# Optimization experiments

Measured on AMD Instinct MI355X. Metric: run time of the kernel, lower is better.

## Reference

```python
import jax, jax.numpy as jnp
import numpy as np

B = 32; H = 56; W = 56; DIM = 384; HEADS = 12; WIN = 7; SHIFT = 3
HEAD_DIM = DIM // HEADS; SCALE = HEAD_DIM ** -0.5
N = WIN * WIN; NW = (H // WIN) * (W // WIN); L = H * W + 1; HID = 4 * DIM


def _rel_index():
    coords = np.stack(np.meshgrid(np.arange(WIN), np.arange(WIN), indexing='ij')).reshape(2, -1)
    rel = (coords[:, :, None] - coords[:, None, :]).transpose(1, 2, 0)
    rel[:, :, 0] += WIN - 1
    rel[:, :, 1] += WIN - 1
    rel[:, :, 0] *= 2 * WIN - 1
    return jnp.asarray(rel.sum(-1))  # (N, N) int


def _attn_mask():
    # standard Swin shift mask, padded with a zero column so the cls key is always visible
    img = np.zeros((H, W))
    sl = (slice(0, -WIN), slice(-WIN, -SHIFT), slice(-SHIFT, None))
    cnt = 0
    for hs in sl:
        for ws in sl:
            img[hs, ws] = cnt
            cnt += 1
    mw = img.reshape(H // WIN, WIN, W // WIN, WIN).transpose(0, 2, 1, 3).reshape(-1, N)
    m = mw[:, None, :] - mw[:, :, None]
    m = np.where(m != 0, -100.0, 0.0).astype(np.float32)
    m = np.pad(m, ((0, 0), (0, 0), (1, 0)))  # (nW, N, N+1)
    return jnp.asarray(m)


REL_INDEX = _rel_index()
ATTN_MASK = _attn_mask()


def _ln(x, g, b, eps=1e-5):
    m = x.mean(-1, keepdims=True)
    v = ((x - m) ** 2).mean(-1, keepdims=True)
    return (x - m) * jax.lax.rsqrt(v + eps) * g + b


def setup_inputs() -> dict:
    key = jax.random.key(0)
    ks = jax.random.split(key, 6)
    s = 0.02
    return dict(
        x=jax.random.normal(ks[0], (B, L, DIM), jnp.float32),
        norm1_g=jnp.ones((DIM,), jnp.float32), norm1_b=jnp.zeros((DIM,), jnp.float32),
        qkv_w=jax.random.normal(ks[1], (3 * DIM, DIM), jnp.float32) * s,
        qkv_b=jnp.zeros((3 * DIM,), jnp.float32),
        rel_bias_table=jax.random.normal(ks[2], ((2 * WIN - 1) ** 2, HEADS), jnp.float32) * s,
        proj_w=jax.random.normal(ks[3], (DIM, DIM), jnp.float32) * s,
        proj_b=jnp.zeros((DIM,), jnp.float32),
        norm2_g=jnp.ones((DIM,), jnp.float32), norm2_b=jnp.zeros((DIM,), jnp.float32),
        fc1_w=jax.random.normal(ks[4], (HID, DIM), jnp.float32) * s,
        fc1_b=jnp.zeros((HID,), jnp.float32),
        fc2_w=jax.random.normal(ks[5], (DIM, HID), jnp.float32) * s,
        fc2_b=jnp.zeros((DIM,), jnp.float32),
    )


def reference(x, norm1_g, norm1_b, qkv_w, qkv_b, rel_bias_table, proj_w, proj_b,
              norm2_g, norm2_b, fc1_w, fc1_b, fc2_w, fc2_b):
    Bx = x.shape[0]
    shortcut = x
    h = _ln(x, norm1_g, norm1_b)
    qkv = h @ qkv_w.T + qkv_b  # (B, L, 3C)

    # ---- global cls attention: token 0 attends to every token (ClsAttention) ----
    t = qkv.reshape(Bx, L, 3, HEADS, HEAD_DIM).transpose(2, 0, 3, 1, 4)  # (3, B, h, L, d)
    q0 = t[0, :, :, 0:1, :] * SCALE
    cls_attn = jax.nn.softmax(jnp.einsum('bhqd,bhkd->bhqk', q0, t[1]), axis=-1)
    cls_out = jnp.einsum('bhqk,bhkd->bhqd', cls_attn, t[2]).transpose(0, 2, 1, 3).reshape(Bx, 1, DIM)

    # ---- shifted-window attention for patch tokens, cls qkv prepended per window ----
    cls_qkv = qkv[:, :1]  # (B, 1, 3C)
    p = qkv[:, 1:].reshape(Bx, H, W, 3 * DIM)
    p = jnp.roll(p, (-SHIFT, -SHIFT), axis=(1, 2))
    pw = p.reshape(Bx, H // WIN, WIN, W // WIN, WIN, 3 * DIM).transpose(0, 1, 3, 2, 4, 5)
    pw = pw.reshape(Bx * NW, N, 3 * DIM)
    cls_rep = jnp.broadcast_to(cls_qkv[:, None], (Bx, NW, 1, 3 * DIM)).reshape(Bx * NW, 1, 3 * DIM)
    qkvw = jnp.concatenate([cls_rep, pw], axis=1)  # (B*nW, N+1, 3C)

    tw = qkvw.reshape(Bx * NW, N + 1, 3, HEADS, HEAD_DIM).transpose(2, 0, 3, 1, 4)
    q = tw[0, :, :, 1:, :] * SCALE  # patch queries (B*nW, h, N, d)
    attn = jnp.einsum('bhqd,bhkd->bhqk', q, tw[1])  # (B*nW, h, N, N+1)
    rel = rel_bias_table[REL_INDEX.reshape(-1)].reshape(N, N, HEADS).transpose(2, 0, 1)
    attn = jnp.concatenate([attn[..., :1], attn[..., 1:] + rel[None]], axis=-1)
    attn = attn.reshape(Bx, NW, HEADS, N, N + 1) + ATTN_MASK[None, :, None]
    attn = jax.nn.softmax(attn.reshape(Bx * NW, HEADS, N, N + 1), axis=-1)
    xw = jnp.einsum('bhqk,bhkd->bhqd', attn, tw[2]).transpose(0, 2, 1, 3).reshape(Bx * NW, N, DIM)

    # window reverse + reverse cyclic shift
    xp = xw.reshape(Bx, H // WIN, W // WIN, WIN, WIN, DIM).transpose(0, 1, 3, 2, 4, 5).reshape(Bx, H, W, DIM)
    xp = jnp.roll(xp, (SHIFT, SHIFT), axis=(1, 2)).reshape(Bx, H * W, DIM)

    a = jnp.concatenate([cls_out, xp], axis=1) @ proj_w.T + proj_b
    x1 = shortcut + a
    h2 = _ln(x1, norm2_g, norm2_b)
    h2 = jax.nn.gelu(h2 @ fc1_w.T + fc1_b, approximate=False)
    return x1 + (h2 @ fc2_w.T + fc2_b)
```

## Files before the change

kernel.cpp:

```cpp
#include <hip/hip_runtime.h>

#define DEVI __device__ __forceinline__

typedef __attribute__((ext_vector_type(8))) __bf16 bf16x8;
typedef __attribute__((ext_vector_type(4))) float f32x4;
typedef unsigned short u16;
typedef unsigned int u32;

static constexpr int kB = 32;
static constexpr int kL = 3137;
static constexpr int kM = kB * kL;
static constexpr int kHeads = 12;
static constexpr float kScale = 0.17677669529663687f;
static constexpr int kNC = 13;

DEVI u16 f2b(float f) {
  u32 u = __float_as_uint(f);
  u32 r = (u + 0x7fffu + ((u >> 16) & 1u)) >> 16;
  return (u16)r;
}
DEVI float blo(u32 u) { return __uint_as_float(u << 16); }
DEVI float bhi(u32 u) { return __uint_as_float(u & 0xffff0000u); }
DEVI float b2f(u16 h) { return __uint_as_float(((u32)h) << 16); }

DEVI void async16(const void* g, void* l) {
  __builtin_amdgcn_global_load_lds((const __attribute__((address_space(1))) u32*)g,
                                   (__attribute__((address_space(3))) u32*)l, 16, 0, 0);
}

DEVI float wred_max(float v) {
#pragma unroll
  for (int o = 32; o; o >>= 1) v = fmaxf(v, __shfl_xor(v, o));
  return v;
}
DEVI float wred_sum(float v) {
#pragma unroll
  for (int o = 32; o; o >>= 1) v += __shfl_xor(v, o);
  return v;
}

__global__ void cvt_all(const float* __restrict__ a, const float* __restrict__ b,
                        const float* __restrict__ c2, const float* __restrict__ d,
                        u16* __restrict__ oa, u16* __restrict__ ob,
                        u16* __restrict__ oc, u16* __restrict__ od) {
  int i = blockIdx.x * 256 + threadIdx.x;
  if (i < 442368) oa[i] = f2b(a[i]);
  else if (i < 589824) ob[i - 442368] = f2b(b[i - 442368]);
  else if (i < 1179648) oc[i - 589824] = f2b(c2[i - 589824]);
  else od[i - 1179648] = f2b(d[i - 1179648]);
}

__global__ __launch_bounds__(256)
void ln384(const float* __restrict__ x, const float* __restrict__ gam,
           const float* __restrict__ bet, u16* __restrict__ out, int rows) {
  int row = blockIdx.x * 4 + (threadIdx.x >> 6);
  if (row >= rows) return;
  int lane = threadIdx.x & 63;
  const float2* xr = (const float2*)(x + (size_t)row * 384);
  float2 v[3];
  float s = 0.f, s2 = 0.f;
#pragma unroll
  for (int i = 0; i < 3; i++) {
    v[i] = xr[lane + 64 * i];
    s += v[i].x + v[i].y;
    s2 += v[i].x * v[i].x + v[i].y * v[i].y;
  }
  s = wred_sum(s);
  s2 = wred_sum(s2);
  float mean = s * (1.f / 384.f);
  float var = s2 * (1.f / 384.f) - mean * mean;
  float rinv = rsqrtf(var + 1e-5f);
  const float2* gp = (const float2*)gam;
  const float2* bp = (const float2*)bet;
  u32* orow = (u32*)(out + (size_t)row * 384);
#pragma unroll
  for (int i = 0; i < 3; i++) {
    int idx = lane + 64 * i;
    float2 gg = gp[idx], bb = bp[idx];
    float lo = (v[i].x - mean) * rinv * gg.x + bb.x;
    float hi = (v[i].y - mean) * rinv * gg.y + bb.y;
    orow[idx] = (u32)f2b(lo) | ((u32)f2b(hi) << 16);
  }
}

DEVI float gelu_exact(float v) { return 0.5f * v * (1.f + erff(v * 0.70710678118654752f)); }

template <int EPI>
__global__ __launch_bounds__(256)
void gemm_bt(const u16* __restrict__ A, const u16* __restrict__ W,
             const float* __restrict__ bias, const float* __restrict__ res,
             void* __restrict__ outp, int M, int N, int K, int NX, int TMv) {
  const int nwg = gridDim.x;
  const int orig = blockIdx.x;
  const int xcd = orig & 7, rest = orig >> 3;
  const int q8 = nwg >> 3, r8 = nwg & 7;
  const int id = ((xcd < r8) ? xcd * (q8 + 1) : r8 * (q8 + 1) + (xcd - r8) * q8) + rest;
  const int col0 = (id % NX) * 128;
  const int rowG = (id / NX) * TMv * 128;

  const int tid = threadIdx.x, lane = tid & 63, wv = tid >> 6;
  __shared__ __align__(16) u16 As[3][128 * 32];
  __shared__ __align__(16) u16 Bs[3][128 * 32];
  const int wm = wv >> 1, wn = wv & 1;
  const int c = lane & 15, g = lane >> 4;
  const int NT = K >> 5;

  const int rr = lane >> 2;
  const int gnat = (lane & 3) ^ ((lane >> 3) & 3);

  auto stage = [&](int t2, int k2, int bfi) {
    int kk = k2 * 32 + gnat * 8;
    int rbase = rowG + t2 * 128;
#pragma unroll
    for (int s = 0; s < 2; s++) {
      int ch = wv * 2 + s;
      int r = ch * 16 + rr;
      async16(A + (size_t)min(rbase + r, M - 1) * K + kk, &As[bfi][ch * 512]);
      async16(W + (size_t)min(col0 + r, N - 1) * K + kk, &Bs[bfi][ch * 512]);
    }
  };

  int cc[4];
  float bv[4];
#pragma unroll
  for (int n = 0; n < 4; n++) {
    cc[n] = col0 + wn * 64 + n * 16 + c;
    bv[n] = bias[cc[n]];
  }

  stage(0, 0, 0);
  stage(0, 1, 1);
  int cur = 0;
  for (int t = 0; t < TMv; ++t) {
    f32x4 acc[4][4];
    f32x4 zero = {0.f, 0.f, 0.f, 0.f};
#pragma unroll
    for (int m = 0; m < 4; m++)
#pragma unroll
      for (int n = 0; n < 4; n++) acc[m][n] = zero;

    for (int kt = 0; kt < NT; ++kt) {
      if (t == TMv - 1 && kt == NT - 1) asm volatile("s_waitcnt vmcnt(0)" ::: "memory");
      else                              asm volatile("s_waitcnt vmcnt(4)" ::: "memory");
      __builtin_amdgcn_s_barrier();
      {
        int kt2 = kt + 2, t2 = t;
        if (kt2 >= NT) { kt2 -= NT; t2++; }
        if (t2 < TMv) {
          int nb = cur + 2; if (nb >= 3) nb -= 3;
          stage(t2, kt2, nb);
        }
      }
      bf16x8 af[4], bw[4];
#pragma unroll
      for (int m = 0; m < 4; m++) {
        int row = wm * 64 + m * 16 + c;
        af[m] = *(const bf16x8*)&As[cur][row * 32 + ((g ^ ((row >> 1) & 3)) << 3)];
      }
#pragma unroll
      for (int n = 0; n < 4; n++) {
        int row = wn * 64 + n * 16 + c;
        bw[n] = *(const bf16x8*)&Bs[cur][row * 32 + ((g ^ ((row >> 1) & 3)) << 3)];
      }
      __builtin_amdgcn_s_setprio(1);
#pragma unroll
      for (int m = 0; m < 4; m++)
#pragma unroll
        for (int n = 0; n < 4; n++)
          acc[m][n] = __builtin_amdgcn_mfma_f32_16x16x32_bf16(af[m], bw[n], acc[m][n], 0, 0, 0);
      __builtin_amdgcn_s_setprio(0);
      cur = cur + 1; if (cur >= 3) cur -= 3;
    }

    int rowT = rowG + t * 128;
#pragma unroll
    for (int m = 0; m < 4; m++) {
      int rb = rowT + wm * 64 + m * 16 + (g << 2);
#pragma unroll
      for (int j = 0; j < 4; j++) {
        int r = rb + j;
        if (r < M) {
#pragma unroll
          for (int n = 0; n < 4; n++) {
            float vv = acc[m][n][j] + bv[n];
            size_t off = (size_t)r * N + cc[n];
            if constexpr (EPI == 0) {
              ((u16*)outp)[off] = f2b(vv);
            } else if constexpr (EPI == 1) {
              ((float*)outp)[off] = vv + res[off];
            } else {
              ((u16*)outp)[off] = f2b(gelu_exact(vv));
            }
          }
        }
      }
    }
  }
}

__global__ __launch_bounds__(256)
void cls_part(const u16* __restrict__ qkv, float* __restrict__ parts) {
  int bh = blockIdx.x;
  int chunk = blockIdx.y;
  int b = bh / kHeads, h = bh % kHeads;
  __shared__ float qs[32];
  __shared__ float ps[256];
  __shared__ float red[8];
  __shared__ float part[8][32];
  int tid = threadIdx.x, lane = tid & 63, wv = tid >> 6;
  size_t rb = (size_t)b * kL;
  if (tid < 32) qs[tid] = b2f(qkv[rb * 1152 + h * 32 + tid]) * kScale;
  __syncthreads();
  int t0 = chunk * 256;
  int nTok = min(256, kL - t0);
  float s = -1e30f;
  if (tid < nTok) {
    const u16* kp = qkv + (rb + t0 + tid) * 1152 + 384 + h * 32;
    s = 0.f;
#pragma unroll
    for (int g4 = 0; g4 < 4; g4++) {
      uint4 u = *(const uint4*)(kp + g4 * 8);
      s += qs[g4*8+0]*blo(u.x) + qs[g4*8+1]*bhi(u.x)
         + qs[g4*8+2]*blo(u.y) + qs[g4*8+3]*bhi(u.y)
         + qs[g4*8+4]*blo(u.z) + qs[g4*8+5]*bhi(u.z)
         + qs[g4*8+6]*blo(u.w) + qs[g4*8+7]*bhi(u.w);
    }
  }
  float m = wred_max(s);
  if (lane == 0) red[wv] = m;
  __syncthreads();
  float gm = fmaxf(fmaxf(red[0], red[1]), fmaxf(red[2], red[3]));
  float p = (tid < nTok) ? __expf(s - gm) : 0.f;
  ps[tid] = p;
  float ls = wred_sum(p);
  if (lane == 0) red[4 + wv] = ls;
  __syncthreads();
  float tot = red[4] + red[5] + red[6] + red[7];
  int d = tid & 31, g = tid >> 5;
  float a = 0.f;
  for (int t = g; t < nTok; t += 8)
    a += ps[t] * b2f(qkv[(rb + t0 + t) * 1152 + 768 + h * 32 + d]);
  part[g][d] = a;
  __syncthreads();
  if (tid < 32) {
    float o = 0.f;
#pragma unroll
    for (int g2 = 0; g2 < 8; g2++) o += part[g2][tid];
    float* pp = parts + ((size_t)bh * kNC + chunk) * 34;
    pp[2 + tid] = o;
    if (tid == 0) { pp[0] = gm; pp[1] = tot; }
  }
}

__global__ __launch_bounds__(64)
void cls_reduce(const float* __restrict__ parts, u16* __restrict__ aout) {
  int bh = blockIdx.x;
  int b = bh / kHeads, h = bh % kHeads;
  int tid = threadIdx.x;
  __shared__ float sm[kNC], ss[kNC];
  if (tid < kNC) {
    sm[tid] = parts[((size_t)bh * kNC + tid) * 34];
    ss[tid] = parts[((size_t)bh * kNC + tid) * 34 + 1];
  }
  __syncthreads();
  float M = -1e30f;
#pragma unroll
  for (int c = 0; c < kNC; c++) M = fmaxf(M, sm[c]);
  float W = 0.f;
#pragma unroll
  for (int c = 0; c < kNC; c++) W += ss[c] * __expf(sm[c] - M);
  if (tid < 32) {
    float o = 0.f;
#pragma unroll
    for (int c = 0; c < kNC; c++)
      o += parts[((size_t)bh * kNC + c) * 34 + 2 + tid] * __expf(sm[c] - M);
    aout[(size_t)b * kL * 384 + h * 32 + tid] = f2b(o / W);
  }
}

__global__ __launch_bounds__(256)
void bias_pre(const float* __restrict__ relb, float* __restrict__ bf) {
  int blk = blockIdx.x;
  int cls = blk / 12, h = blk % 12;
  int clsH = (cls >> 1) & 1, clsW = cls & 1;
  for (int idx = threadIdx.x; idx < 4096; idx += 256) {
    int k = idx >> 6, q = idx & 63;
    float v = 0.f;
    if (k >= 50) {
      v = -1e9f;
    } else if (k >= 1 && q < 49) {
      int kt = k - 1, ki = kt / 7, kj = kt % 7;
      int qi = q / 7, qj = q % 7;
      v = relb[((qi - ki + 6) * 13 + (qj - kj + 6)) * 12 + h];
      int rq = (clsH ? (qi < 4 ? 1 : 2) : 0) * 3 + (clsW ? (qj < 4 ? 1 : 2) : 0);
      int rk = (clsH ? (ki < 4 ? 1 : 2) : 0) * 3 + (clsW ? (kj < 4 ? 1 : 2) : 0);
      if (rq != rk) v -= 100.f;
    }
    bf[(size_t)blk * 4096 + idx] = v;
  }
}

__global__ __launch_bounds__(256)
void win_attn2(const u16* __restrict__ qkv, const float* __restrict__ biasf,
               u16* __restrict__ aout) {
  const int tid = threadIdx.x, lane = tid & 63, wv = tid >> 6;
  const int gid = blockIdx.x * 4 + wv;
  const int h = gid % 12;
  const int wr = gid / 12;
  const int win = wr & 63, b = wr >> 6;
  const int wi = win >> 3, wj = win & 7;
  const int cls = ((wi == 7) ? 2 : 0) + ((wj == 7) ? 1 : 0);
  const int c = lane & 15, g = lane >> 4;

  __shared__ __align__(16) u16 KS[4][64 * 40];
  __shared__ __align__(16) u16 VT[4][32 * 72];
  __shared__ int RW[4][52];
  u16* Ks = KS[wv];
  u16* Vt = VT[wv];
  int* Rows = RW[wv];

#pragma unroll
  for (int it = 0; it < 2; ++it) {
    int idx = it * 64 + lane;
    int tok = idx >> 1, half = idx & 1;
    if (tok < 50) {
      int row;
      if (tok == 0) {
        row = b * kL;
      } else {
        int n = tok - 1;
        int i = n / 7, j = n % 7;
        int r = wi * 7 + i, c2 = wj * 7 + j;
        int orr = r + 3; if (orr >= 56) orr -= 56;
        int occ = c2 + 3; if (occ >= 56) occ -= 56;
        row = b * kL + 1 + orr * 56 + occ;
      }
      if (half == 0) Rows[tok] = row;
      const u16* base = qkv + (size_t)row * 1152 + h * 32 + half * 16;
      uint4 k0 = *(const uint4*)(base + 384);
      uint4 k1 = *(const uint4*)(base + 384 + 8);
      *(uint4*)&Ks[tok * 40 + half * 16] = k0;
      *(uint4*)&Ks[tok * 40 + half * 16 + 8] = k1;
      uint4 v0 = *(const uint4*)(base + 768);
      uint4 v1 = *(const uint4*)(base + 768 + 8);
      u32 vw[8] = {v0.x, v0.y, v0.z, v0.w, v1.x, v1.y, v1.z, v1.w};
#pragma unroll
      for (int m = 0; m < 8; ++m) {
        Vt[(half * 16 + m * 2 + 0) * 72 + tok] = (u16)(vw[m] & 0xffffu);
        Vt[(half * 16 + m * 2 + 1) * 72 + tok] = (u16)(vw[m] >> 16);
      }
    } else {
      uint4 z = {0u, 0u, 0u, 0u};
      *(uint4*)&Ks[tok * 40 + half * 16] = z;
      *(uint4*)&Ks[tok * 40 + half * 16 + 8] = z;
#pragma unroll
      for (int m = 0; m < 16; ++m) Vt[(half * 16 + m) * 72 + tok] = 0;
    }
  }
  __syncthreads();

  bf16x8 qf[4];
#pragma unroll
  for (int nt = 0; nt < 4; ++nt) {
    int q = nt * 16 + c;
    if (q > 48) q = 48;
    const u16* qp = qkv + (size_t)Rows[q + 1] * 1152 + h * 32 + g * 8;
    qf[nt] = *(const bf16x8*)qp;
  }

  f32x4 s[4][4];
  {
    f32x4 z = {0.f, 0.f, 0.f, 0.f};
    bf16x8 kf[4];
#pragma unroll
    for (int mt = 0; mt < 4; ++mt)
      kf[mt] = *(const bf16x8*)&Ks[(mt * 16 + c) * 40 + g * 8];
#pragma unroll
    for (int mt = 0; mt < 4; ++mt)
#pragma unroll
      for (int nt = 0; nt < 4; ++nt)
        s[mt][nt] = __builtin_amdgcn_mfma_f32_16x16x32_bf16(kf[mt], qf[nt], z, 0, 0, 0);
  }

  const float* bp = biasf + (size_t)(cls * 12 + h) * 4096;
  u32 wq[4][8];
#pragma unroll
  for (int nt = 0; nt < 4; ++nt) {
    float pv[16];
#pragma unroll
    for (int mt = 0; mt < 4; ++mt)
#pragma unroll
      for (int r = 0; r < 4; ++r)
        pv[mt * 4 + r] = s[mt][nt][r] * kScale + bp[(mt * 16 + g * 4 + r) * 64 + nt * 16 + c];
    float mx = pv[0];
#pragma unroll
    for (int i2 = 1; i2 < 16; ++i2) mx = fmaxf(mx, pv[i2]);
    mx = fmaxf(mx, __shfl_xor(mx, 16));
    mx = fmaxf(mx, __shfl_xor(mx, 32));
    float sum = 0.f;
#pragma unroll
    for (int i2 = 0; i2 < 16; ++i2) { pv[i2] = __expf(pv[i2] - mx); sum += pv[i2]; }
    sum += __shfl_xor(sum, 16);
    sum += __shfl_xor(sum, 32);
    float rs = 1.f / sum;
#pragma unroll
    for (int i2 = 0; i2 < 16; ++i2) pv[i2] *= rs;
#pragma unroll
    for (int mt = 0; mt < 4; ++mt) {
      u32 w0, w1;
      asm("v_cvt_pk_bf16_f32 %0, %1, %2" : "=v"(w0) : "v"(pv[mt * 4 + 0]), "v"(pv[mt * 4 + 1]));
      asm("v_cvt_pk_bf16_f32 %0, %1, %2" : "=v"(w1) : "v"(pv[mt * 4 + 2]), "v"(pv[mt * 4 + 3]));
      wq[nt][mt * 2 + 0] = w0;
      wq[nt][mt * 2 + 1] = w1;
    }
  }

  bf16x8 pa[4][2];
#pragma unroll
  for (int mt2 = 0; mt2 < 4; ++mt2)
#pragma unroll
    for (int ks = 0; ks < 2; ++ks) {
      union { u32 u[4]; bf16x8 v; } cvt;
#pragma unroll
      for (int wj2 = 0; wj2 < 4; ++wj2) {
        int srcLane = c + 16 * (((g & 1) << 1) + (wj2 >> 1));
        u32 a0 = (u32)__shfl((int)wq[mt2][(2 * ks + 0) * 2 + (wj2 & 1)], srcLane);
        u32 a1 = (u32)__shfl((int)wq[mt2][(2 * ks + 1) * 2 + (wj2 & 1)], srcLane);
        cvt.u[wj2] = (g < 2) ? a0 : a1;
      }
      pa[mt2][ks] = cvt.v;
    }

  f32x4 o[4][2];
  f32x4 z2 = {0.f, 0.f, 0.f, 0.f};
#pragma unroll
  for (int mt2 = 0; mt2 < 4; ++mt2)
#pragma unroll
    for (int ntd = 0; ntd < 2; ++ntd) o[mt2][ntd] = z2;
#pragma unroll
  for (int ks = 0; ks < 2; ++ks) {
    bf16x8 vf[2];
#pragma unroll
    for (int ntd = 0; ntd < 2; ++ntd)
      vf[ntd] = *(const bf16x8*)&Vt[(ntd * 16 + c) * 72 + ks * 32 + g * 8];
#pragma unroll
    for (int mt2 = 0; mt2 < 4; ++mt2)
#pragma unroll
      for (int ntd = 0; ntd < 2; ++ntd)
        o[mt2][ntd] = __builtin_amdgcn_mfma_f32_16x16x32_bf16(pa[mt2][ks], vf[ntd], o[mt2][ntd], 0, 0, 0);
  }

#pragma unroll
  for (int mt2 = 0; mt2 < 4; ++mt2)
#pragma unroll
    for (int r = 0; r < 4; ++r) {
      int q = mt2 * 16 + g * 4 + r;
      if (q < 49) {
        int row = Rows[q + 1];
        u16* op = aout + (size_t)row * 384 + h * 32 + c;
        op[0]  = f2b(o[mt2][0][r]);
        op[16] = f2b(o[mt2][1][r]);
      }
    }
}

extern "C" void kernel_launch(void* const* d_in, const int* in_sizes, int n_in,
                              void* d_out, int out_size, void* d_ws, size_t ws_size,
                              hipStream_t stream) {
  const float* x      = (const float*)d_in[0];
  const float* n1g    = (const float*)d_in[1];
  const float* n1b    = (const float*)d_in[2];
  const float* qkv_w  = (const float*)d_in[3];
  const float* qkv_b  = (const float*)d_in[4];
  const float* relb   = (const float*)d_in[5];
  const float* proj_w = (const float*)d_in[6];
  const float* proj_b = (const float*)d_in[7];
  const float* n2g    = (const float*)d_in[8];
  const float* n2b    = (const float*)d_in[9];
  const float* fc1_w  = (const float*)d_in[10];
  const float* fc1_b  = (const float*)d_in[11];
  const float* fc2_w  = (const float*)d_in[12];
  const float* fc2_b  = (const float*)d_in[13];
  float* out = (float*)d_out;
  char* ws = (char*)d_ws;

  u16* wqkv  = (u16*)(ws + 0);
  float* biasf = (float*)(ws + 0);
  u16* wproj = (u16*)(ws + 884736);
  u16* wfc1  = (u16*)(ws + 1179648);
  u16* wfc2  = (u16*)(ws + 2359296);
  u16* qkvb  = (u16*)(ws + 3538944);
  u16* h2b   = (u16*)(ws + 3538944);
  u16* gb    = (u16*)(ws + 3538944 + 41943040);
  u16* hbuf  = (u16*)(ws + 234823680);
  float* parts = (float*)d_out;

  cvt_all<<<6912, 256, 0, stream>>>(qkv_w, proj_w, fc1_w, fc2_w, wqkv, wproj, wfc1, wfc2);

  ln384<<<(kM + 3) / 4, 256, 0, stream>>>(x, n1g, n1b, hbuf, kM);
  gemm_bt<0><<<9 * 197, 256, 0, stream>>>(hbuf, wqkv, qkv_b, nullptr, qkvb, kM, 1152, 384, 9, 4);
  bias_pre<<<48, 256, 0, stream>>>(relb, biasf);
  cls_part<<<dim3(kB * kHeads, kNC), 256, 0, stream>>>(qkvb, parts);
  cls_reduce<<<kB * kHeads, 64, 0, stream>>>(parts, hbuf);
  win_attn2<<<kB * 64 * kHeads / 4, 256, 0, stream>>>(qkvb, biasf, hbuf);
  gemm_bt<1><<<3 * 393, 256, 0, stream>>>(hbuf, wproj, proj_b, x, out, kM, 384, 384, 3, 2);

  for (int c = 0; c < 2; c++) {
    int r0 = c * 50192, nr = 50192;
    ln384<<<(nr + 3) / 4, 256, 0, stream>>>(out + (size_t)r0 * 384, n2g, n2b, h2b, nr);
    gemm_bt<2><<<12 * 99, 256, 0, stream>>>(h2b, wfc1, fc1_b, nullptr, gb, nr, 1536, 384, 12, 4);
    gemm_bt<1><<<3 * 393, 256, 0, stream>>>(gb, wfc2, fc2_b, out + (size_t)r0 * 384,
                                            out + (size_t)r0 * 384, nr, 384, 1536, 3, 1);
  }
}
```

Measured before the change: 1.004 ms.

## Replace 128x128 GEMM with 256x256-tile 512-thread double-buffered GEMM

Every GEMM (qkv, proj, fc1, fc2) now uses a new kernel with 256x256 output tiles and 8 waves per block. Each wave holds an 8x4 set of MFMA accumulators. K is staged in 64-wide steps split into two 32-wide halves, with double-buffered LDS and loads interleaved between MFMA phases. The larger tile is meant to raise arithmetic intensity and cut global/L2 traffic per FLOP. In exchange it adds register pressure, wasted work on N not divisible by 256 (1152, 384 need column guards), and fewer blocks for occupancy.

After: 1.539 ms. 53.3% more time.

```diff
diff --git a/kernel.cpp b/kernel.cpp
--- a/kernel.cpp
+++ b/kernel.cpp
@@ -86,102 +86,160 @@
 DEVI float gelu_exact(float v) { return 0.5f * v * (1.f + erff(v * 0.70710678118654752f)); }
 
 template <int EPI>
-__global__ __launch_bounds__(256)
-void gemm_bt(const u16* __restrict__ A, const u16* __restrict__ W,
+__global__ __launch_bounds__(512, 2)
+void gemm256(const u16* __restrict__ A, const u16* __restrict__ W,
              const float* __restrict__ bias, const float* __restrict__ res,
-             void* __restrict__ outp, int M, int N, int K, int NX, int TMv) {
+             void* __restrict__ outp, int M, int N, int K, int NXS) {
   const int nwg = gridDim.x;
   const int orig = blockIdx.x;
   const int xcd = orig & 7, rest = orig >> 3;
   const int q8 = nwg >> 3, r8 = nwg & 7;
   const int id = ((xcd < r8) ? xcd * (q8 + 1) : r8 * (q8 + 1) + (xcd - r8) * q8) + rest;
-  const int col0 = (id % NX) * 128;
-  const int rowG = (id / NX) * TMv * 128;
+  const int col0 = (id % NXS) * 256, row0 = (id / NXS) * 256;
 
   const int tid = threadIdx.x, lane = tid & 63, wv = tid >> 6;
-  __shared__ __align__(16) u16 As[3][128 * 32];
-  __shared__ __align__(16) u16 Bs[3][128 * 32];
-  const int wm = wv >> 1, wn = wv & 1;
   const int c = lane & 15, g = lane >> 4;
-  const int NT = K >> 5;
+  const int wr = wv >> 2, wc = wv & 3;
+
+  __shared__ __align__(16) u16 As[2][2][8192];
+  __shared__ __align__(16) u16 Bs[2][2][8192];
+
+  f32x4 acc[8][4];
+  f32x4 zero = {0.f, 0.f, 0.f, 0.f};
+#pragma unroll
+  for (int m = 0; m < 8; m++)
+#pragma unroll
+    for (int n = 0; n < 4; n++) acc[m][n] = zero;
 
   const int rr = lane >> 2;
-  const int gnat = (lane & 3) ^ ((lane >> 3) & 3);
-
-  auto stage = [&](int t2, int k2, int bfi) {
-    int kk = k2 * 32 + gnat * 8;
-    int rbase = rowG + t2 * 128;
-#pragma unroll
-    for (int s = 0; s < 2; s++) {
-      int ch = wv * 2 + s;
-      int r = ch * 16 + rr;
-      async16(A + (size_t)min(rbase + r, M - 1) * K + kk, &As[bfi][ch * 512]);
-      async16(W + (size_t)min(col0 + r, N - 1) * K + kk, &Bs[bfi][ch * 512]);
-    }
+  const int gsrc = (lane & 3) ^ ((lane >> 3) & 3);
+  const u16* baseA[2];
+  const u16* baseB[2];
+#pragma unroll
+  for (int s = 0; s < 2; s++) {
+    int i = wv * 2 + s;
+    baseA[s] = A + (size_t)min(row0 + i * 16 + rr, M - 1) * K + gsrc * 8;
+    baseB[s] = W + (size_t)min(col0 + i * 16 + rr, N - 1) * K + gsrc * 8;
+  }
+
+  auto stageA = [&](int kt, int kh) {
+    int off = kt * 64 + kh * 32;
+    int d = kt & 1;
+#pragma unroll
+    for (int s = 0; s < 2; s++)
+      async16(baseA[s] + off, &As[d][kh][(wv * 2 + s) * 512]);
   };
+  auto stageB = [&](int kt, int kh) {
+    int off = kt * 64 + kh * 32;
+    int d = kt & 1;
+#pragma unroll
+    for (int s = 0; s < 2; s++)
+      async16(baseB[s] + off, &Bs[d][kh][(wv * 2 + s) * 512]);
+  };
+
+  const int axor = ((g ^ ((c >> 1) & 3)) << 3);
+
+  const int NKT = K >> 6;
+  stageA(0, 0); stageB(0, 0); stageA(0, 1); stageB(0, 1);
+
+  for (int kt = 0; kt < NKT; ++kt) {
+    const int d = kt & 1;
+    const bool pf = (kt + 1 < NKT);
+    bf16x8 af[4], bw[4];
+
+    asm volatile("s_waitcnt vmcnt(4)" ::: "memory");
+    __builtin_amdgcn_s_barrier();
+#pragma unroll
+    for (int m = 0; m < 4; m++) {
+      int r = wr * 128 + m * 16 + c;
+      af[m] = *(const bf16x8*)&As[d][0][r * 32 + axor];
+    }
+#pragma unroll
+    for (int n = 0; n < 4; n++) {
+      int r = wc * 64 + n * 16 + c;
+      bw[n] = *(const bf16x8*)&Bs[d][0][r * 32 + axor];
+    }
+    if (pf) stageA(kt + 1, 0);
+    __builtin_amdgcn_s_setprio(1);
+#pragma unroll
+    for (int m = 0; m < 4; m++)
+#pragma unroll
+      for (int n = 0; n < 4; n++)
+        acc[m][n] = __builtin_amdgcn_mfma_f32_16x16x32_bf16(af[m], bw[n], acc[m][n], 0, 0, 0);
+    __builtin_amdgcn_s_setprio(0);
+    __builtin_amdgcn_s_barrier();
+
+#pragma unroll
+    for (int m = 0; m < 4; m++) {
+      int r = wr * 128 + (m + 4) * 16 + c;
+      af[m] = *(const bf16x8*)&As[d][0][r * 32 + axor];
+    }
+    if (pf) stageB(kt + 1, 0);
+    __builtin_amdgcn_s_setprio(1);
+#pragma unroll
+    for (int m = 0; m < 4; m++)
+#pragma unroll
+      for (int n = 0; n < 4; n++)
+        acc[m + 4][n] = __builtin_amdgcn_mfma_f32_16x16x32_bf16(af[m], bw[n], acc[m + 4][n], 0, 0, 0);
+    __builtin_amdgcn_s_setprio(0);
+    __builtin_amdgcn_s_barrier();
+
+    if (pf) asm volatile("s_waitcnt vmcnt(4)" ::: "memory");
+    else    asm volatile("s_waitcnt vmcnt(0)" ::: "memory");
+    __builtin_amdgcn_s_barrier();
+#pragma unroll
+    for (int m = 0; m < 4; m++) {
+      int r = wr * 128 + m * 16 + c;
+      af[m] = *(const bf16x8*)&As[d][1][r * 32 + axor];
+    }
+#pragma unroll
+    for (int n = 0; n < 4; n++) {
+      int r = wc * 64 + n * 16 + c;
+      bw[n] = *(const bf16x8*)&Bs[d][1][r * 32 + axor];
+    }
+    if (pf) stageA(kt + 1, 1);
+    __builtin_amdgcn_s_setprio(1);
+#pragma unroll
+    for (int m = 0; m < 4; m++)
+#pragma unroll
+      for (int n = 0; n < 4; n++)
+        acc[m][n] = __builtin_amdgcn_mfma_f32_16x16x32_bf16(af[m], bw[n], acc[m][n], 0, 0, 0);
+    __builtin_amdgcn_s_setprio(0);
+    __builtin_amdgcn_s_barrier();
+
+#pragma unroll
+    for (int m = 0; m < 4; m++) {
+      int r = wr * 128 + (m + 4) * 16 + c;
+      af[m] = *(const bf16x8*)&As[d][1][r * 32 + axor];
+    }
+    if (pf) stageB(kt + 1, 1);
+    __builtin_amdgcn_s_setprio(1);
+#pragma unroll
+    for (int m = 0; m < 4; m++)
+#pragma unroll
+      for (int n = 0; n < 4; n++)
+        acc[m + 4][n] = __builtin_amdgcn_mfma_f32_16x16x32_bf16(af[m], bw[n], acc[m + 4][n], 0, 0, 0);
+    __builtin_amdgcn_s_setprio(0);
+    __builtin_amdgcn_s_barrier();
+  }
 
   int cc[4];
   float bv[4];
 #pragma unroll
   for (int n = 0; n < 4; n++) {
-    cc[n] = col0 + wn * 64 + n * 16 + c;
-    bv[n] = bias[cc[n]];
-  }
-
-  stage(0, 0, 0);
-  stage(0, 1, 1);
-  int cur = 0;
-  for (int t = 0; t < TMv; ++t) {
-    f32x4 acc[4][4];
-    f32x4 zero = {0.f, 0.f, 0.f, 0.f};
-#pragma unroll
-    for (int m = 0; m < 4; m++)
-#pragma unroll
-      for (int n = 0; n < 4; n++) acc[m][n] = zero;
-
-    for (int kt = 0; kt < NT; ++kt) {
-      if (t == TMv - 1 && kt == NT - 1) asm volatile("s_waitcnt vmcnt(0)" ::: "memory");
-      else                              asm volatile("s_waitcnt vmcnt(4)" ::: "memory");
-      __builtin_amdgcn_s_barrier();
-      {
-        int kt2 = kt + 2, t2 = t;
-        if (kt2 >= NT) { kt2 -= NT; t2++; }
-        if (t2 < TMv) {
-          int nb = cur + 2; if (nb >= 3) nb -= 3;
-          stage(t2, kt2, nb);
-        }
-      }
-      bf16x8 af[4], bw[4];
-#pragma unroll
-      for (int m = 0; m < 4; m++) {
-        int row = wm * 64 + m * 16 + c;
-        af[m] = *(const bf16x8*)&As[cur][row * 32 + ((g ^ ((row >> 1) & 3)) << 3)];
-      }
-#pragma unroll
-      for (int n = 0; n < 4; n++) {
-        int row = wn * 64 + n * 16 + c;
-        bw[n] = *(const bf16x8*)&Bs[cur][row * 32 + ((g ^ ((row >> 1) & 3)) << 3)];
-      }
-      __builtin_amdgcn_s_setprio(1);
-#pragma unroll
-      for (int m = 0; m < 4; m++)
-#pragma unroll
-        for (int n = 0; n < 4; n++)
-          acc[m][n] = __builtin_amdgcn_mfma_f32_16x16x32_bf16(af[m], bw[n], acc[m][n], 0, 0, 0);
-      __builtin_amdgcn_s_setprio(0);
-      cur = cur + 1; if (cur >= 3) cur -= 3;
-    }
-
-    int rowT = rowG + t * 128;
-#pragma unroll
-    for (int m = 0; m < 4; m++) {
-      int rb = rowT + wm * 64 + m * 16 + (g << 2);
-#pragma unroll
-      for (int j = 0; j < 4; j++) {
-        int r = rb + j;
-        if (r < M) {
-#pragma unroll
-          for (int n = 0; n < 4; n++) {
+    cc[n] = col0 + wc * 64 + n * 16 + c;
+    bv[n] = (cc[n] < N) ? bias[cc[n]] : 0.f;
+  }
+#pragma unroll
+  for (int m = 0; m < 8; m++) {
+    int rb = row0 + wr * 128 + m * 16 + (g << 2);
+#pragma unroll
+    for (int j = 0; j < 4; j++) {
+      int r = rb + j;
+      if (r < M) {
+#pragma unroll
+        for (int n = 0; n < 4; n++) {
+          if (cc[n] < N) {
             float vv = acc[m][n][j] + bv[n];
             size_t off = (size_t)r * N + cc[n];
             if constexpr (EPI == 0) {
@@ -498,18 +556,18 @@
   cvt_all<<<6912, 256, 0, stream>>>(qkv_w, proj_w, fc1_w, fc2_w, wqkv, wproj, wfc1, wfc2);
 
   ln384<<<(kM + 3) / 4, 256, 0, stream>>>(x, n1g, n1b, hbuf, kM);
-  gemm_bt<0><<<9 * 197, 256, 0, stream>>>(hbuf, wqkv, qkv_b, nullptr, qkvb, kM, 1152, 384, 9, 4);
+  gemm256<0><<<393 * 5, 512, 0, stream>>>(hbuf, wqkv, qkv_b, nullptr, qkvb, kM, 1152, 384, 5);
   bias_pre<<<48, 256, 0, stream>>>(relb, biasf);
   cls_part<<<dim3(kB * kHeads, kNC), 256, 0, stream>>>(qkvb, parts);
   cls_reduce<<<kB * kHeads, 64, 0, stream>>>(parts, hbuf);
   win_attn2<<<kB * 64 * kHeads / 4, 256, 0, stream>>>(qkvb, biasf, hbuf);
-  gemm_bt<1><<<3 * 393, 256, 0, stream>>>(hbuf, wproj, proj_b, x, out, kM, 384, 384, 3, 2);
+  gemm256<1><<<393 * 2, 512, 0, stream>>>(hbuf, wproj, proj_b, x, out, kM, 384, 384, 2);
 
   for (int c = 0; c < 2; c++) {
     int r0 = c * 50192, nr = 50192;
     ln384<<<(nr + 3) / 4, 256, 0, stream>>>(out + (size_t)r0 * 384, n2g, n2b, h2b, nr);
-    gemm_bt<2><<<12 * 99, 256, 0, stream>>>(h2b, wfc1, fc1_b, nullptr, gb, nr, 1536, 384, 12, 4);
-    gemm_bt<1><<<3 * 393, 256, 0, stream>>>(gb, wfc2, fc2_b, out + (size_t)r0 * 384,
-                                            out + (size_t)r0 * 384, nr, 384, 1536, 3, 1);
-  }
-}
+    gemm256<2><<<197 * 6, 512, 0, stream>>>(h2b, wfc1, fc1_b, nullptr, gb, nr, 1536, 384, 6);
+    gemm256<1><<<197 * 2, 512, 0, stream>>>(gb, wfc2, fc2_b, out + (size_t)r0 * 384,
+                                            out + (size_t)r0 * 384, nr, 384, 1536, 2);
+  }
+}
```
